# Performance work log

Measured on AMD Instinct MI355X. Metric: run time of the kernel, lower is better.

## Reference

```python
import jax, jax.numpy as jnp
import numpy as np

# Synaptic (snntorch) constants: alpha = exp(-dt/tau_s), beta = exp(-dt/tau_m)
DT, TAU_S, TAU_M = 1.0, 5.0, 10.0
ALPHA = float(np.exp(-DT / TAU_S))
BETA = float(np.exp(-DT / TAU_M))
THRESH = 1.0


def heaviside(u):
    return (u > 0).astype(u.dtype)


def setup_inputs() -> dict:
    key = jax.random.key(0)
    k1, k2 = jax.random.split(key)
    T, B, D1, D2 = 128, 256, 1024, 512
    inp = jax.random.uniform(k1, (T, B, D1), dtype=jnp.float32)
    # kaiming_normal_ on [d2, d1] (fan_in = d1), then * mu (=1.0)
    w = jax.random.normal(k2, (D2, D1), dtype=jnp.float32) * np.float32(np.sqrt(2.0 / D1))
    return {"input": inp, "weight": w}


def reference(input, weight):
    T, B = input.shape[0], input.shape[1]
    D2 = weight.shape[0]
    # step i (i=1..T-1) consumes F.linear(input[i-1], W); batch all GEMMs at once
    cur = jnp.einsum('tbi,oi->tbo', input[:-1], weight)  # [T-1, B, D2]

    def step(carry, c):
        syn, mem = carry
        reset = heaviside(mem - THRESH)          # spike from previous membrane
        syn = ALPHA * syn + c                    # synaptic current decay + drive
        mem = (BETA * mem + syn) * (1.0 - reset)  # zero-reset membrane update
        spk = heaviside(mem - THRESH)
        return (syn, mem), (spk, mem, syn)

    zeros = jnp.zeros((B, D2), input.dtype)
    _, (spk, V, I) = jax.lax.scan(step, (zeros, zeros), cur)

    z0 = jnp.zeros((1, B, D2), input.dtype)  # outputs at t=0 stay zero
    output = jnp.concatenate([z0, spk], axis=0)
    V = jnp.concatenate([z0, V], axis=0)
    I = jnp.concatenate([z0, I], axis=0)
    return output, V, I
```

## Files before the change

kernel.cpp:

```cpp
#include <hip/hip_runtime.h>
#include <cstddef>
#include <cstdint>

#define TT 128
#define BB 256
#define D1 1024
#define D2 512
#define SS (BB * D2)
#define MM (127 * BB)

#define ALPHA 0.8187307530779818f
#define BETA  0.9048374180359595f

typedef _Float16 half8 __attribute__((ext_vector_type(8)));
typedef float floatx16 __attribute__((ext_vector_type(16)));

__global__ __launch_bounds__(256) void convert_w(const float* __restrict__ W,
                                                 _Float16* __restrict__ Whi,
                                                 _Float16* __restrict__ Wlo) {
    const int T = blockIdx.x * 256 + threadIdx.x;
    const int l = T & 63;
    const int ch = (T >> 6) & 7;
    const int nB = (T >> 9) & 3;
    const int kt = T >> 11;
    const int row = nB * 128 + (ch & 3) * 32 + (l & 31);
    const int k = kt * 32 + (ch >> 2) * 16 + (l >> 5) * 8;
    const float* src = W + (size_t)row * D1 + k;
    float4 w0 = *(const float4*)src;
    float4 w1 = *(const float4*)(src + 4);
    float f[8] = {w0.x, w0.y, w0.z, w0.w, w1.x, w1.y, w1.z, w1.w};
    half8 hi, lo;
#pragma unroll
    for (int j = 0; j < 8; ++j) {
        _Float16 h = (_Float16)f[j];
        hi[j] = h;
        lo[j] = (_Float16)((f[j] - (float)h) * 2048.0f);
    }
    *(half8*)(Whi + (size_t)T * 8) = hi;
    *(half8*)(Wlo + (size_t)T * 8) = lo;
}

#define GLOAD16(gp, lp)                                                        \
    __builtin_amdgcn_global_load_lds(                                          \
        (const __attribute__((address_space(1))) void*)(gp),                   \
        (__attribute__((address_space(3))) void*)(lp), 16, 0, 0)

__global__ __launch_bounds__(512, 2) void gemm_mfma(const float* __restrict__ A,
                                                    const _Float16* __restrict__ Whi,
                                                    const _Float16* __restrict__ Wlo,
                                                    float* __restrict__ C) {
    __shared__ _Float16 lds[2][4][4096];

    const int tid = threadIdx.x;
    const int lane = tid & 63;
    const int w = tid >> 6;
    const int wm = w >> 2;
    const int wn = w & 3;
    const int bm = blockIdx.x * 128;
    const int nB = blockIdx.y;
    const int bn = nB * 128;
    const int m_ = lane & 31;
    const int q = lane >> 5;

    const int o_ = tid & 3;
    const int r0 = tid >> 2;
    const int chA = ((o_ >> 1) << 2) + (r0 >> 5);
    const int sA = chA * 512 + ((o_ & 1) * 32 + (r0 & 31)) * 8;
    const float* Ab0 = A + (size_t)(bm + r0) * D1 + o_ * 8;

    const _Float16* WsrcH = Whi + (size_t)nB * 4096 + w * 512 + lane * 8;
    const _Float16* WsrcL = Wlo + (size_t)nB * 4096 + w * 512 + lane * 8;

    const int fA0 = (wm * 2 + 0) * 512 + lane * 8;
    const int fA1 = (wm * 2 + 1) * 512 + lane * 8;
    const int fB = wn * 512 + lane * 8;

    floatx16 accm[2], accl[2];
    accm[0] = (floatx16)0.0f; accm[1] = (floatx16)0.0f;
    accl[0] = (floatx16)0.0f; accl[1] = (floatx16)0.0f;

    float4 ra0, ra1;
    float4 rb0, rb1;

#define STAGE_A(BUF, F0, F1)                                                   \
    {                                                                          \
        float fv[8] = {F0.x, F0.y, F0.z, F0.w, F1.x, F1.y, F1.z, F1.w};        \
        half8 hh, ll;                                                          \
        _Pragma("unroll")                                                      \
        for (int u = 0; u < 8; ++u) {                                          \
            _Float16 hv = (_Float16)fv[u];                                     \
            hh[u] = hv;                                                        \
            ll[u] = (_Float16)((fv[u] - (float)hv) * 2048.0f);                 \
        }                                                                      \
        *(half8*)&lds[BUF][0][sA] = hh;                                        \
        *(half8*)&lds[BUF][1][sA] = ll;                                        \
    }

#define MFMA6(BUF, KS)                                                         \
    {                                                                          \
        const half8 ah0 = *(const half8*)&lds[BUF][0][fA0 + (KS)*2048];        \
        const half8 ah1 = *(const half8*)&lds[BUF][0][fA1 + (KS)*2048];        \
        const half8 al0 = *(const half8*)&lds[BUF][1][fA0 + (KS)*2048];        \
        const half8 al1 = *(const half8*)&lds[BUF][1][fA1 + (KS)*2048];        \
        const half8 bh = *(const half8*)&lds[BUF][2][fB + (KS)*2048];          \
        const half8 bl = *(const half8*)&lds[BUF][3][fB + (KS)*2048];          \
        accm[0] = __builtin_amdgcn_mfma_f32_32x32x16_f16(ah0, bh, accm[0], 0, 0, 0); \
        accl[0] = __builtin_amdgcn_mfma_f32_32x32x16_f16(ah0, bl, accl[0], 0, 0, 0); \
        accl[0] = __builtin_amdgcn_mfma_f32_32x32x16_f16(al0, bh, accl[0], 0, 0, 0); \
        accm[1] = __builtin_amdgcn_mfma_f32_32x32x16_f16(ah1, bh, accm[1], 0, 0, 0); \
        accl[1] = __builtin_amdgcn_mfma_f32_32x32x16_f16(ah1, bl, accl[1], 0, 0, 0); \
        accl[1] = __builtin_amdgcn_mfma_f32_32x32x16_f16(al1, bh, accl[1], 0, 0, 0); \
    }

#define BODY(JT, BUF, C0, C1, N0, N1, PREF_A, VMN)                             \
    {                                                                          \
        asm volatile("" ::: "memory");                 \
        GLOAD16(WsrcH + (size_t)((JT) + 1) * 16384, &lds[(BUF) ^ 1][2][w * 512]); \
        GLOAD16(WsrcL + (size_t)((JT) + 1) * 16384, &lds[(BUF) ^ 1][3][w * 512]); \
        __builtin_amdgcn_sched_barrier(0);     \
        if (PREF_A) {                                                          \
            const int kf = ((JT) + 2) * 32;                                    \
            N0 = *(const float4*)(Ab0 + kf);                                   \
            N1 = *(const float4*)(Ab0 + kf + 4);                               \
        }                                                                      \
        STAGE_A((BUF) ^ 1, C0, C1);                                            \
        __builtin_amdgcn_s_setprio(1);                                         \
        MFMA6(BUF, 0);                                                         \
        __builtin_amdgcn_s_setprio(0);                                         \
        __builtin_amdgcn_s_setprio(1);                                         \
        MFMA6(BUF, 1);                                                         \
        __builtin_amdgcn_s_setprio(0);                                         \
        asm volatile("s_waitcnt vmcnt(" #VMN ") lgkmcnt(0)" ::: "memory");     \
        __builtin_amdgcn_s_barrier();                                          \
    }

    GLOAD16(WsrcH, &lds[0][2][w * 512]);
    GLOAD16(WsrcL, &lds[0][3][w * 512]);
    __builtin_amdgcn_sched_barrier(0);
    ra0 = *(const float4*)(Ab0);
    ra1 = *(const float4*)(Ab0 + 4);
    rb0 = *(const float4*)(Ab0 + 32);
    rb1 = *(const float4*)(Ab0 + 36);
    STAGE_A(0, ra0, ra1);
    asm volatile("s_waitcnt vmcnt(2) lgkmcnt(0)" ::: "memory");
    __builtin_amdgcn_s_barrier();

    for (int jj = 0; jj < 30; jj += 2) {
        BODY(jj, 0, rb0, rb1, ra0, ra1, 1, 2)
        BODY(jj + 1, 1, ra0, ra1, rb0, rb1, 1, 2)
    }
    BODY(30, 0, rb0, rb1, ra0, ra1, 0, 0)
    asm volatile("" ::: "memory");
    __builtin_amdgcn_s_setprio(1);
    MFMA6(1, 0);
    __builtin_amdgcn_s_setprio(0);
    __builtin_amdgcn_s_setprio(1);
    MFMA6(1, 1);
    __builtin_amdgcn_s_setprio(0);

#undef BODY
#undef MFMA6
#undef STAGE_A

    const int n = bn + wn * 32 + m_;
#pragma unroll
    for (int mb = 0; mb < 2; ++mb) {
#pragma unroll
        for (int reg = 0; reg < 16; ++reg) {
            const int row = (reg & 3) + 8 * (reg >> 2) + 4 * q;
            const int m = bm + wm * 64 + mb * 32 + row;
            C[(size_t)m * D2 + n] = accm[mb][reg] + accl[mb][reg] * (1.0f / 2048.0f);
        }
    }
}

__global__ __launch_bounds__(256) void scan_kernel(float* __restrict__ out) {
    const int j = blockIdx.x * 256 + threadIdx.x;
    float* spk = out;
    float* V = out + TT * SS;
    float* I = out + 2 * TT * SS;

    spk[j] = 0.0f;
    V[j] = 0.0f;
    I[j] = 0.0f;

    float syn = 0.0f, mem = 0.0f;

#define STEP(tt, cc)                                     \
    {                                                    \
        const float reset = (mem > 1.0f) ? 1.0f : 0.0f;  \
        syn = ALPHA * syn + (cc);                        \
        mem = (BETA * mem + syn) * (1.0f - reset);       \
        const int idx = (tt) * SS + j;                   \
        spk[idx] = (mem > 1.0f) ? 1.0f : 0.0f;           \
        V[idx] = mem;                                    \
        I[idx] = syn;                                    \
    }

    float c0 = I[1 * SS + j];
    float c1 = I[2 * SS + j];
    float c2 = I[3 * SS + j];
    float c3 = I[4 * SS + j];

    int t = 1;
    for (; t <= 117; t += 4) {
        const float n0 = I[(t + 4) * SS + j];
        const float n1 = I[(t + 5) * SS + j];
        const float n2 = I[(t + 6) * SS + j];
        const float n3 = I[(t + 7) * SS + j];
        STEP(t + 0, c0);
        STEP(t + 1, c1);
        STEP(t + 2, c2);
        STEP(t + 3, c3);
        c0 = n0; c1 = n1; c2 = n2; c3 = n3;
    }
    {
        const float n0 = I[125 * SS + j];
        const float n1 = I[126 * SS + j];
        const float n2 = I[127 * SS + j];
        STEP(121, c0);
        STEP(122, c1);
        STEP(123, c2);
        STEP(124, c3);
        STEP(125, n0);
        STEP(126, n1);
        STEP(127, n2);
    }
#undef STEP
}

extern "C" void kernel_launch(void* const* d_in, const int* in_sizes, int n_in,
                              void* d_out, int out_size, void* d_ws, size_t ws_size,
                              hipStream_t stream) {
    const float* input = (const float*)d_in[0];
    const float* weight = (const float*)d_in[1];
    float* out = (float*)d_out;

    _Float16* Whi = (_Float16*)(out + SS);
    _Float16* Wlo = Whi + (size_t)D2 * D1;

    float* Cdst = out + (size_t)2 * TT * SS + SS;

    convert_w<<<dim3((D2 * D1 / 8) / 256), dim3(256), 0, stream>>>(weight, Whi, Wlo);
    gemm_mfma<<<dim3(MM / 128, D2 / 128), dim3(512), 0, stream>>>(input, Whi, Wlo, Cdst);
    scan_kernel<<<dim3(SS / 256), dim3(256), 0, stream>>>(out);
}
```

Baseline: 391.7 us.

## Widen GEMM tile to 128x256 and reorder grid so N-blocks share A rows

Each workgroup now computes a 128x256 output tile instead of 128x128, so every wave holds a 2x2 block of MFMA accumulators. The fp32 A tile is loaded and split into hi/lo halves half as often. The weight layout in the convert kernel is reindexed to match. The grid is swapped so the two N-blocks for the same M rows are adjacent, which should improve L2 reuse of A. The cost is a doubled accumulator count with more register pressure, more LDS per block that may hurt the two-blocks-per-CU occupancy, and half as many blocks.

After: 387.4 us. Within noise of the previous version (-1.1%).

```diff
diff --git a/kernel.cpp b/kernel.cpp
--- a/kernel.cpp
+++ b/kernel.cpp
@@ -20,11 +20,11 @@
                                                  _Float16* __restrict__ Wlo) {
     const int T = blockIdx.x * 256 + threadIdx.x;
     const int l = T & 63;
-    const int ch = (T >> 6) & 7;
-    const int nB = (T >> 9) & 3;
+    const int ch = (T >> 6) & 15;
+    const int nB = (T >> 10) & 1;
     const int kt = T >> 11;
-    const int row = nB * 128 + (ch & 3) * 32 + (l & 31);
-    const int k = kt * 32 + (ch >> 2) * 16 + (l >> 5) * 8;
+    const int row = nB * 256 + (ch & 7) * 32 + (l & 31);
+    const int k = kt * 32 + (ch >> 3) * 16 + (l >> 5) * 8;
     const float* src = W + (size_t)row * D1 + k;
     float4 w0 = *(const float4*)src;
     float4 w1 = *(const float4*)(src + 4);
@@ -40,6 +40,12 @@
     *(half8*)(Wlo + (size_t)T * 8) = lo;
 }
 
+#define AHo 0
+#define ALo 4096
+#define WHo 8192
+#define WLo 16384
+#define BUFSZ 24576
+
 #define GLOAD16(gp, lp)                                                        \
     __builtin_amdgcn_global_load_lds(                                          \
         (const __attribute__((address_space(1))) void*)(gp),                   \
@@ -49,35 +55,41 @@
                                                     const _Float16* __restrict__ Whi,
                                                     const _Float16* __restrict__ Wlo,
                                                     float* __restrict__ C) {
-    __shared__ _Float16 lds[2][4][4096];
+    __shared__ _Float16 lds[2][BUFSZ];
 
     const int tid = threadIdx.x;
     const int lane = tid & 63;
     const int w = tid >> 6;
     const int wm = w >> 2;
     const int wn = w & 3;
-    const int bm = blockIdx.x * 128;
-    const int nB = blockIdx.y;
-    const int bn = nB * 128;
+    const int nB = blockIdx.x;
+    const int bm = blockIdx.y * 128;
+    const int bn = nB * 256;
     const int m_ = lane & 31;
     const int q = lane >> 5;
 
     const int o_ = tid & 3;
     const int r0 = tid >> 2;
-    const int chA = ((o_ >> 1) << 2) + (r0 >> 5);
-    const int sA = chA * 512 + ((o_ & 1) * 32 + (r0 & 31)) * 8;
+    const int sA = (((o_ >> 1) << 2) + (r0 >> 5)) * 512 +
+                   ((o_ & 1) * 32 + (r0 & 31)) * 8;
     const float* Ab0 = A + (size_t)(bm + r0) * D1 + o_ * 8;
 
-    const _Float16* WsrcH = Whi + (size_t)nB * 4096 + w * 512 + lane * 8;
-    const _Float16* WsrcL = Wlo + (size_t)nB * 4096 + w * 512 + lane * 8;
+    const _Float16* WsrcH = Whi + (size_t)nB * 8192 + (2 * w) * 512 + lane * 8;
+    const _Float16* WsrcL = Wlo + (size_t)nB * 8192 + (2 * w) * 512 + lane * 8;
 
     const int fA0 = (wm * 2 + 0) * 512 + lane * 8;
     const int fA1 = (wm * 2 + 1) * 512 + lane * 8;
-    const int fB = wn * 512 + lane * 8;
-
-    floatx16 accm[2], accl[2];
-    accm[0] = (floatx16)0.0f; accm[1] = (floatx16)0.0f;
-    accl[0] = (floatx16)0.0f; accl[1] = (floatx16)0.0f;
+    const int fB0 = (wn * 2 + 0) * 512 + lane * 8;
+    const int fB1 = (wn * 2 + 1) * 512 + lane * 8;
+
+    floatx16 accm[2][2], accl[2][2];
+#pragma unroll
+    for (int i = 0; i < 2; ++i)
+#pragma unroll
+        for (int j = 0; j < 2; ++j) {
+            accm[i][j] = (floatx16)0.0f;
+            accl[i][j] = (floatx16)0.0f;
+        }
 
     float4 ra0, ra1;
     float4 rb0, rb1;
@@ -92,31 +104,41 @@
             hh[u] = hv;                                                        \
             ll[u] = (_Float16)((fv[u] - (float)hv) * 2048.0f);                 \
         }                                                                      \
-        *(half8*)&lds[BUF][0][sA] = hh;                                        \
-        *(half8*)&lds[BUF][1][sA] = ll;                                        \
-    }
-
-#define MFMA6(BUF, KS)                                                         \
+        *(half8*)&lds[BUF][AHo + sA] = hh;                                     \
+        *(half8*)&lds[BUF][ALo + sA] = ll;                                     \
+    }
+
+#define MFMA12(BUF, KS)                                                        \
     {                                                                          \
-        const half8 ah0 = *(const half8*)&lds[BUF][0][fA0 + (KS)*2048];        \
-        const half8 ah1 = *(const half8*)&lds[BUF][0][fA1 + (KS)*2048];        \
-        const half8 al0 = *(const half8*)&lds[BUF][1][fA0 + (KS)*2048];        \
-        const half8 al1 = *(const half8*)&lds[BUF][1][fA1 + (KS)*2048];        \
-        const half8 bh = *(const half8*)&lds[BUF][2][fB + (KS)*2048];          \
-        const half8 bl = *(const half8*)&lds[BUF][3][fB + (KS)*2048];          \
-        accm[0] = __builtin_amdgcn_mfma_f32_32x32x16_f16(ah0, bh, accm[0], 0, 0, 0); \
-        accl[0] = __builtin_amdgcn_mfma_f32_32x32x16_f16(ah0, bl, accl[0], 0, 0, 0); \
-        accl[0] = __builtin_amdgcn_mfma_f32_32x32x16_f16(al0, bh, accl[0], 0, 0, 0); \
-        accm[1] = __builtin_amdgcn_mfma_f32_32x32x16_f16(ah1, bh, accm[1], 0, 0, 0); \
-        accl[1] = __builtin_amdgcn_mfma_f32_32x32x16_f16(ah1, bl, accl[1], 0, 0, 0); \
-        accl[1] = __builtin_amdgcn_mfma_f32_32x32x16_f16(al1, bh, accl[1], 0, 0, 0); \
+        const half8 ah0 = *(const half8*)&lds[BUF][AHo + fA0 + (KS)*2048];     \
+        const half8 ah1 = *(const half8*)&lds[BUF][AHo + fA1 + (KS)*2048];     \
+        const half8 al0 = *(const half8*)&lds[BUF][ALo + fA0 + (KS)*2048];     \
+        const half8 al1 = *(const half8*)&lds[BUF][ALo + fA1 + (KS)*2048];     \
+        const half8 bh0 = *(const half8*)&lds[BUF][WHo + fB0 + (KS)*4096];     \
+        const half8 bh1 = *(const half8*)&lds[BUF][WHo + fB1 + (KS)*4096];     \
+        const half8 bl0 = *(const half8*)&lds[BUF][WLo + fB0 + (KS)*4096];     \
+        const half8 bl1 = *(const half8*)&lds[BUF][WLo + fB1 + (KS)*4096];     \
+        accm[0][0] = __builtin_amdgcn_mfma_f32_32x32x16_f16(ah0, bh0, accm[0][0], 0, 0, 0); \
+        accm[0][1] = __builtin_amdgcn_mfma_f32_32x32x16_f16(ah0, bh1, accm[0][1], 0, 0, 0); \
+        accm[1][0] = __builtin_amdgcn_mfma_f32_32x32x16_f16(ah1, bh0, accm[1][0], 0, 0, 0); \
+        accm[1][1] = __builtin_amdgcn_mfma_f32_32x32x16_f16(ah1, bh1, accm[1][1], 0, 0, 0); \
+        accl[0][0] = __builtin_amdgcn_mfma_f32_32x32x16_f16(ah0, bl0, accl[0][0], 0, 0, 0); \
+        accl[0][1] = __builtin_amdgcn_mfma_f32_32x32x16_f16(ah0, bl1, accl[0][1], 0, 0, 0); \
+        accl[1][0] = __builtin_amdgcn_mfma_f32_32x32x16_f16(ah1, bl0, accl[1][0], 0, 0, 0); \
+        accl[1][1] = __builtin_amdgcn_mfma_f32_32x32x16_f16(ah1, bl1, accl[1][1], 0, 0, 0); \
+        accl[0][0] = __builtin_amdgcn_mfma_f32_32x32x16_f16(al0, bh0, accl[0][0], 0, 0, 0); \
+        accl[0][1] = __builtin_amdgcn_mfma_f32_32x32x16_f16(al0, bh1, accl[0][1], 0, 0, 0); \
+        accl[1][0] = __builtin_amdgcn_mfma_f32_32x32x16_f16(al1, bh0, accl[1][0], 0, 0, 0); \
+        accl[1][1] = __builtin_amdgcn_mfma_f32_32x32x16_f16(al1, bh1, accl[1][1], 0, 0, 0); \
     }
 
 #define BODY(JT, BUF, C0, C1, N0, N1, PREF_A, VMN)                             \
     {                                                                          \
         asm volatile("" ::: "memory");                 \
-        GLOAD16(WsrcH + (size_t)((JT) + 1) * 16384, &lds[(BUF) ^ 1][2][w * 512]); \
-        GLOAD16(WsrcL + (size_t)((JT) + 1) * 16384, &lds[(BUF) ^ 1][3][w * 512]); \
+        GLOAD16(WsrcH + (size_t)((JT) + 1) * 16384,       &lds[(BUF) ^ 1][WHo + 2 * w * 512]);      \
+        GLOAD16(WsrcH + (size_t)((JT) + 1) * 16384 + 512, &lds[(BUF) ^ 1][WHo + (2 * w + 1) * 512]);\
+        GLOAD16(WsrcL + (size_t)((JT) + 1) * 16384,       &lds[(BUF) ^ 1][WLo + 2 * w * 512]);      \
+        GLOAD16(WsrcL + (size_t)((JT) + 1) * 16384 + 512, &lds[(BUF) ^ 1][WLo + (2 * w + 1) * 512]);\
         __builtin_amdgcn_sched_barrier(0);     \
         if (PREF_A) {                                                          \
             const int kf = ((JT) + 2) * 32;                                    \
@@ -125,17 +147,19 @@
         }                                                                      \
         STAGE_A((BUF) ^ 1, C0, C1);                                            \
         __builtin_amdgcn_s_setprio(1);                                         \
-        MFMA6(BUF, 0);                                                         \
+        MFMA12(BUF, 0);                                                        \
         __builtin_amdgcn_s_setprio(0);                                         \
         __builtin_amdgcn_s_setprio(1);                                         \
-        MFMA6(BUF, 1);                                                         \
+        MFMA12(BUF, 1);                                                        \
         __builtin_amdgcn_s_setprio(0);                                         \
         asm volatile("s_waitcnt vmcnt(" #VMN ") lgkmcnt(0)" ::: "memory");     \
         __builtin_amdgcn_s_barrier();                                          \
     }
 
-    GLOAD16(WsrcH, &lds[0][2][w * 512]);
-    GLOAD16(WsrcL, &lds[0][3][w * 512]);
+    GLOAD16(WsrcH,       &lds[0][WHo + 2 * w * 512]);
+    GLOAD16(WsrcH + 512, &lds[0][WHo + (2 * w + 1) * 512]);
+    GLOAD16(WsrcL,       &lds[0][WLo + 2 * w * 512]);
+    GLOAD16(WsrcL + 512, &lds[0][WLo + (2 * w + 1) * 512]);
     __builtin_amdgcn_sched_barrier(0);
     ra0 = *(const float4*)(Ab0);
     ra1 = *(const float4*)(Ab0 + 4);
@@ -152,26 +176,29 @@
     BODY(30, 0, rb0, rb1, ra0, ra1, 0, 0)
     asm volatile("" ::: "memory");
     __builtin_amdgcn_s_setprio(1);
-    MFMA6(1, 0);
+    MFMA12(1, 0);
     __builtin_amdgcn_s_setprio(0);
     __builtin_amdgcn_s_setprio(1);
-    MFMA6(1, 1);
+    MFMA12(1, 1);
     __builtin_amdgcn_s_setprio(0);
 
 #undef BODY
-#undef MFMA6
+#undef MFMA12
 #undef STAGE_A
 
-    const int n = bn + wn * 32 + m_;
-#pragma unroll
-    for (int mb = 0; mb < 2; ++mb) {
-#pragma unroll
-        for (int reg = 0; reg < 16; ++reg) {
-            const int row = (reg & 3) + 8 * (reg >> 2) + 4 * q;
-            const int m = bm + wm * 64 + mb * 32 + row;
-            C[(size_t)m * D2 + n] = accm[mb][reg] + accl[mb][reg] * (1.0f / 2048.0f);
+#pragma unroll
+    for (int mb = 0; mb < 2; ++mb)
+#pragma unroll
+        for (int nb = 0; nb < 2; ++nb) {
+            const int n = bn + wn * 64 + nb * 32 + m_;
+#pragma unroll
+            for (int reg = 0; reg < 16; ++reg) {
+                const int row = (reg & 3) + 8 * (reg >> 2) + 4 * q;
+                const int m = bm + wm * 64 + mb * 32 + row;
+                C[(size_t)m * D2 + n] =
+                    accm[mb][nb][reg] + accl[mb][nb][reg] * (1.0f / 2048.0f);
+            }
         }
-    }
 }
 
 __global__ __launch_bounds__(256) void scan_kernel(float* __restrict__ out) {
@@ -242,6 +269,6 @@
     float* Cdst = out + (size_t)2 * TT * SS + SS;
 
     convert_w<<<dim3((D2 * D1 / 8) / 256), dim3(256), 0, stream>>>(weight, Whi, Wlo);
-    gemm_mfma<<<dim3(MM / 128, D2 / 128), dim3(512), 0, stream>>>(input, Whi, Wlo, Cdst);
+    gemm_mfma<<<dim3(2, MM / 128), dim3(512), 0, stream>>>(input, Whi, Wlo, Cdst);
     scan_kernel<<<dim3(SS / 256), dim3(256), 0, stream>>>(out);
 }
```
